# Kernel optimization log

Measured on AMD Instinct MI355X. Metric: run time of the kernel, lower is better.

## Reference

```python
import jax, jax.numpy as jnp
import numpy as np

INF = jnp.float32(np.inf)
LAMBDA_VAL = 1.0
NUM_CLASSES = 10

def setup_inputs() -> dict:
    key = jax.random.key(0)
    k1, k2, k3 = jax.random.split(key, 3)
    N, P, D = 65536, 2048, 64
    x = jax.random.normal(k1, (N, D), dtype=jnp.float32)
    y = jax.random.randint(k2, (N,), 0, NUM_CLASSES)
    prototypes = jax.random.normal(k3, (P, D), dtype=jnp.float32)
    prototype_labels = jnp.arange(P) % NUM_CLASSES
    return {"x": x, "y": y, "prototypes": prototypes, "prototype_labels": prototype_labels}

def _cdist(x, p):
    # Euclidean pairwise distances via the gemm expansion (matches torch.cdist default
    x2 = jnp.sum(x * x, axis=1, keepdims=True)          # [N, 1]
    p2 = jnp.sum(p * p, axis=1)                          # [P]
    sq = x2 + p2[None, :] - 2.0 * (x @ p.T)              # [N, P]
    return jnp.sqrt(jnp.maximum(sq, 0.0))

def reference(x, y, prototypes, prototype_labels):
    distances = _cdist(x, prototypes)                    # [N, P]
    same = prototype_labels[None, :] == y[:, None]       # [N, P] bool
    pos = jnp.min(jnp.where(same, distances, INF), axis=1)   # [N]
    neg = jnp.min(jnp.where(~same, distances, INF), axis=1)  # [N]
    mu = (pos - neg) / (pos + neg)
    loss = jnp.mean(jax.nn.sigmoid(LAMBDA_VAL * mu))
    return loss
```

## Files before the change

### kernel.cpp

```cpp
#include <hip/hip_runtime.h>
#include <math.h>

#define NROWS  65536
#define DDIM   64
#define NCLS   10

#define CLS_SLOTS   208
#define CLS_FFRAGS  13
#define CLS_STRIDE  27648
#define CLS_P2_OFF  26624

typedef __attribute__((ext_vector_type(8))) short bf16x8;
typedef __attribute__((ext_vector_type(4))) float f32x4;
typedef __attribute__((ext_vector_type(4))) unsigned int u32x4;

__device__ inline unsigned int f2bf(float f) {
    unsigned int u = __float_as_uint(f);
    return (u + 0x7FFFu + ((u >> 16) & 1u)) >> 16;
}

template <int CTRL>
__device__ inline float rorMin(float v) {
    int t = __builtin_amdgcn_update_dpp(0, __float_as_int(v), CTRL, 0xF, 0xF, false);
    return fminf(v, __int_as_float(t));
}

__global__ __launch_bounds__(256) void prep_kernel(
        const float* __restrict__ protos, char* __restrict__ wsB,
        float* __restrict__ out) {
    int t = blockIdx.x * 256 + threadIdx.x;
    int s = t >> 3, jj = t & 7;
    int L = s / CLS_SLOTS;
    int j = s - L * CLS_SLOTS;
    int cnt = (L < 8) ? 205 : 204;
    bool real = (j < cnt);
    float v[8] = {0.f, 0.f, 0.f, 0.f, 0.f, 0.f, 0.f, 0.f};
    if (real) {
        const float* src = protos + (L + 10 * j) * DDIM + jj * 8;
        float4 a = *(const float4*)src;
        float4 b = *(const float4*)(src + 4);
        v[0] = a.x; v[1] = a.y; v[2] = a.z; v[3] = a.w;
        v[4] = b.x; v[5] = b.y; v[6] = b.z; v[7] = b.w;
    }
    float ss = 0.f;
#pragma unroll
    for (int i = 0; i < 8; i++) ss = fmaf(v[i], v[i], ss);
    ss += __shfl_xor(ss, 1, 64);
    ss += __shfl_xor(ss, 2, 64);
    ss += __shfl_xor(ss, 4, 64);
    unsigned int w[4];
#pragma unroll
    for (int i = 0; i < 4; i++) {
        unsigned int lo = f2bf(-2.f * v[2 * i]);
        unsigned int hi = f2bf(-2.f * v[2 * i + 1]);
        w[i] = lo | (hi << 16);
    }
    size_t base = (size_t)L * CLS_STRIDE;
    *(u32x4*)(wsB + base + (size_t)(j * 8 + (jj ^ (j & 7))) * 16) =
        (u32x4){w[0], w[1], w[2], w[3]};
    if (jj == 0)
        *(float*)(wsB + base + CLS_P2_OFF + j * 4) =
            real ? ss : __builtin_inff();
    if (t == 0) out[0] = 0.f;
}

template <int CI>
__device__ __forceinline__ void classBody(
        const char* __restrict__ base0,
        int b0off, int b1off, int p2off,
        bf16x8 (&pb0)[3], bf16x8 (&pb1)[3], float (&pp2)[3],
        bf16x8 (&afrag)[4][2], float (&mMin)[4][4]) {
    const char* base = base0 + CI * CLS_STRIDE;
#pragma unroll
    for (int f = 0; f < CLS_FFRAGS; f++) {
        const int slot = (CI * CLS_FFRAGS + f) % 3;
        bf16x8 b0 = pb0[slot];
        bf16x8 b1 = pb1[slot];
        float p2v = pp2[slot];
        if (f <= CLS_FFRAGS - 4) {
            pb0[slot] = *(const bf16x8*)(base + (f + 3) * 2048 + b0off);
            pb1[slot] = *(const bf16x8*)(base + (f + 3) * 2048 + b1off);
            pp2[slot] = *(const float*)(base + p2off + (f + 3) * 64);
        } else if (CI < 4) {
            const char* nb = base + CLS_STRIDE;
            pb0[slot] = *(const bf16x8*)(nb + (f - 10) * 2048 + b0off);
            pb1[slot] = *(const bf16x8*)(nb + (f - 10) * 2048 + b1off);
            pp2[slot] = *(const float*)(nb + p2off + (f - 10) * 64);
        }
        f32x4 p2f = (f32x4){p2v, p2v, p2v, p2v};
#pragma unroll
        for (int m = 0; m < 4; m++) {
            f32x4 acc = __builtin_amdgcn_mfma_f32_16x16x32_bf16(
                afrag[m][0], b0, p2f, 0, 0, 0);
            acc = __builtin_amdgcn_mfma_f32_16x16x32_bf16(
                afrag[m][1], b1, acc, 0, 0, 0);
#pragma unroll
            for (int r = 0; r < 4; r++)
                mMin[m][r] = fminf(mMin[m][r], acc[r]);
        }
    }
}

__global__ __launch_bounds__(256, 2) void glvq_fused(
        const float* __restrict__ x, const int* __restrict__ y,
        const char* __restrict__ wsB, float* __restrict__ out) {
    __shared__ float ldsX2[2][64];
    __shared__ float ldsPos[2][64];
    __shared__ float ldsNeg[2][64];
    __shared__ float ldsRed[2];

    const int tid  = threadIdx.x;
    const int wave = tid >> 6;
    const int lane = tid & 63;
    const int quad = lane >> 4;
    const int l15  = lane & 15;
    const int pair = wave >> 1;
    const int h    = wave & 1;
    const float CINF = __builtin_inff();
    const int rowBase = blockIdx.x * 128 + pair * 64;

    const int b0off = l15 * 128 + (quad ^ (l15 & 7)) * 16;
    const int b1off = l15 * 128 + ((4 + quad) ^ (l15 & 7)) * 16;
    const int p2off = CLS_P2_OFF + l15 * 4;

    const char* base0 = wsB + (size_t)(h * 5) * CLS_STRIDE;

    bf16x8 pb0[3], pb1[3];
    float  pp2[3];
#pragma unroll
    for (int f = 0; f < 3; f++) {
        pb0[f] = *(const bf16x8*)(base0 + f * 2048 + b0off);
        pb1[f] = *(const bf16x8*)(base0 + f * 2048 + b1off);
        pp2[f] = *(const float*)(base0 + p2off + f * 64);
    }

    bf16x8 afrag[4][2];
#pragma unroll
    for (int m = 0; m < 4; m++) {
        float ss = 0.f;
#pragma unroll
        for (int k = 0; k < 2; k++) {
            const float* src = x + (size_t)(rowBase + m * 16 + l15) * DDIM + k * 32 + quad * 8;
            float4 a = *(const float4*)src;
            float4 b = *(const float4*)(src + 4);
            float v[8] = {a.x, a.y, a.z, a.w, b.x, b.y, b.z, b.w};
            unsigned int w[4];
#pragma unroll
            for (int i = 0; i < 4; i++) {
                ss = fmaf(v[2 * i],     v[2 * i],     ss);
                ss = fmaf(v[2 * i + 1], v[2 * i + 1], ss);
                w[i] = f2bf(v[2 * i]) | (f2bf(v[2 * i + 1]) << 16);
            }
            union { u32x4 u; bf16x8 hh; } cvt;
            cvt.u = (u32x4){w[0], w[1], w[2], w[3]};
            afrag[m][k] = cvt.hh;
        }
        ss += __shfl_xor(ss, 16, 64);
        ss += __shfl_xor(ss, 32, 64);
        if (h == 0 && quad == 0) ldsX2[pair][m * 16 + l15] = ss;
    }

    unsigned int yp[4];
#pragma unroll
    for (int m = 0; m < 4; m++) {
        int4 yl = *(const int4*)(y + rowBase + m * 16 + quad * 4);
        yp[m] = (unsigned)yl.x | ((unsigned)yl.y << 8) |
                ((unsigned)yl.z << 16) | ((unsigned)yl.w << 24);
    }

    float pos[4][4], neg[4][4], mMin[4][4];
#pragma unroll
    for (int m = 0; m < 4; m++)
#pragma unroll
        for (int r = 0; r < 4; r++) {
            pos[m][r] = -CINF;
            neg[m][r] = CINF;
            mMin[m][r] = CINF;
        }

    auto endClass = [&](int cls) {
#pragma unroll
        for (int m = 0; m < 4; m++)
#pragma unroll
            for (int r = 0; r < 4; r++) {
                float vmin = mMin[m][r];
                vmin = rorMin<0x128>(vmin);
                vmin = rorMin<0x124>(vmin);
                vmin = rorMin<0x122>(vmin);
                vmin = rorMin<0x121>(vmin);
                bool isPos = (((yp[m] >> (8 * r)) & 255u) == (unsigned)cls);
                pos[m][r] = isPos ? vmin : pos[m][r];
                neg[m][r] = isPos ? neg[m][r] : fminf(neg[m][r], vmin);
                mMin[m][r] = CINF;
            }
    };

    const int h5 = h * 5;
    classBody<0>(base0, b0off, b1off, p2off, pb0, pb1, pp2, afrag, mMin); endClass(h5 + 0);
    classBody<1>(base0, b0off, b1off, p2off, pb0, pb1, pp2, afrag, mMin); endClass(h5 + 1);
    classBody<2>(base0, b0off, b1off, p2off, pb0, pb1, pp2, afrag, mMin); endClass(h5 + 2);
    classBody<3>(base0, b0off, b1off, p2off, pb0, pb1, pp2, afrag, mMin); endClass(h5 + 3);
    classBody<4>(base0, b0off, b1off, p2off, pb0, pb1, pp2, afrag, mMin); endClass(h5 + 4);

    if (h == 1 && l15 == 0) {
#pragma unroll
        for (int m = 0; m < 4; m++)
#pragma unroll
            for (int r = 0; r < 4; r++) {
                ldsPos[pair][m * 16 + quad * 4 + r] = pos[m][r];
                ldsNeg[pair][m * 16 + quad * 4 + r] = neg[m][r];
            }
    }
    __syncthreads();

    float sum = 0.f;
    if (h == 0 && l15 == 0) {
#pragma unroll
        for (int m = 0; m < 4; m++)
#pragma unroll
            for (int r = 0; r < 4; r++) {
                int row = m * 16 + quad * 4 + r;
                float p = fmaxf(pos[m][r], ldsPos[pair][row]);
                float n = fminf(neg[m][r], ldsNeg[pair][row]);
                float x2v = ldsX2[pair][row];
                float sp = sqrtf(fmaxf(x2v + p, 0.f));
                float sn = sqrtf(fmaxf(x2v + n, 0.f));
                float mu = (sp - sn) / (sp + sn);
                sum += 1.f / (1.f + __expf(-mu));
            }
    }
    sum += __shfl_xor(sum, 16, 64);
    sum += __shfl_xor(sum, 32, 64);
    if (h == 0 && lane == 0) ldsRed[pair] = sum;
    __syncthreads();
    if (tid == 0)
        atomicAdd(out, (ldsRed[0] + ldsRed[1]) * (1.f / (float)NROWS));
}

extern "C" void kernel_launch(void* const* d_in, const int* in_sizes, int n_in,
                              void* d_out, int out_size, void* d_ws, size_t ws_size,
                              hipStream_t stream) {
    const float* x      = (const float*)d_in[0];
    const int*   yp     = (const int*)d_in[1];
    const float* protos = (const float*)d_in[2];
    float* out = (float*)d_out;
    char*  wsB = (char*)d_ws;

    prep_kernel<<<65, 256, 0, stream>>>(protos, wsB, out);
    glvq_fused<<<512, 256, 0, stream>>>(x, yp, wsB, out);
}
```

Before: 96.70 us.

## Split prototype fragments within each class across wave pair instead of splitting classes

Previously each of the two waves in a pair handled five whole classes (13 fragments each). Now each wave handles half the fragments of all ten classes (7 fragments per class), using a 4-deep register prefetch ring instead of 3. Per-class minima go to shared memory, and after a barrier one wave per pair combines them per row with the label and computes the loss. This changes load balance and prefetch depth but adds shared-memory traffic, and 2×7 fragments exceed the original 13, so one fragment per class appears to be processed twice; that is harmless for a minimum if the data is valid.

```diff
diff --git a/kernel.cpp b/kernel.cpp
--- a/kernel.cpp
+++ b/kernel.cpp
@@ -66,26 +66,28 @@
 
 template <int CI>
 __device__ __forceinline__ void classBody(
-        const char* __restrict__ base0,
+        const char* __restrict__ wsB, int fLo,
         int b0off, int b1off, int p2off,
-        bf16x8 (&pb0)[3], bf16x8 (&pb1)[3], float (&pp2)[3],
+        bf16x8 (&pb0)[4], bf16x8 (&pb1)[4], float (&pp2)[4],
         bf16x8 (&afrag)[4][2], float (&mMin)[4][4]) {
-    const char* base = base0 + CI * CLS_STRIDE;
-#pragma unroll
-    for (int f = 0; f < CLS_FFRAGS; f++) {
-        const int slot = (CI * CLS_FFRAGS + f) % 3;
+    const char* base = wsB + (size_t)CI * CLS_STRIDE;
+#pragma unroll
+    for (int i = 0; i < 7; i++) {
+        const int slot = (CI * 7 + i) & 3;
         bf16x8 b0 = pb0[slot];
         bf16x8 b1 = pb1[slot];
         float p2v = pp2[slot];
-        if (f <= CLS_FFRAGS - 4) {
-            pb0[slot] = *(const bf16x8*)(base + (f + 3) * 2048 + b0off);
-            pb1[slot] = *(const bf16x8*)(base + (f + 3) * 2048 + b1off);
-            pp2[slot] = *(const float*)(base + p2off + (f + 3) * 64);
-        } else if (CI < 4) {
+        if (i < 3) {
+            const int f = fLo + i + 4;
+            pb0[slot] = *(const bf16x8*)(base + f * 2048 + b0off);
+            pb1[slot] = *(const bf16x8*)(base + f * 2048 + b1off);
+            pp2[slot] = *(const float*)(base + p2off + f * 64);
+        } else if (CI < NCLS - 1) {
             const char* nb = base + CLS_STRIDE;
-            pb0[slot] = *(const bf16x8*)(nb + (f - 10) * 2048 + b0off);
-            pb1[slot] = *(const bf16x8*)(nb + (f - 10) * 2048 + b1off);
-            pp2[slot] = *(const float*)(nb + p2off + (f - 10) * 64);
+            const int f = fLo + i - 3;
+            pb0[slot] = *(const bf16x8*)(nb + f * 2048 + b0off);
+            pb1[slot] = *(const bf16x8*)(nb + f * 2048 + b1off);
+            pp2[slot] = *(const float*)(nb + p2off + f * 64);
         }
         f32x4 p2f = (f32x4){p2v, p2v, p2v, p2v};
 #pragma unroll
@@ -104,9 +106,8 @@
 __global__ __launch_bounds__(256, 2) void glvq_fused(
         const float* __restrict__ x, const int* __restrict__ y,
         const char* __restrict__ wsB, float* __restrict__ out) {
+    __shared__ float ldsMin[2][2][NCLS][64];
     __shared__ float ldsX2[2][64];
-    __shared__ float ldsPos[2][64];
-    __shared__ float ldsNeg[2][64];
     __shared__ float ldsRed[2];
 
     const int tid  = threadIdx.x;
@@ -118,20 +119,20 @@
     const int h    = wave & 1;
     const float CINF = __builtin_inff();
     const int rowBase = blockIdx.x * 128 + pair * 64;
+    const int fLo = h * 6;
 
     const int b0off = l15 * 128 + (quad ^ (l15 & 7)) * 16;
     const int b1off = l15 * 128 + ((4 + quad) ^ (l15 & 7)) * 16;
     const int p2off = CLS_P2_OFF + l15 * 4;
 
-    const char* base0 = wsB + (size_t)(h * 5) * CLS_STRIDE;
-
-    bf16x8 pb0[3], pb1[3];
-    float  pp2[3];
-#pragma unroll
-    for (int f = 0; f < 3; f++) {
-        pb0[f] = *(const bf16x8*)(base0 + f * 2048 + b0off);
-        pb1[f] = *(const bf16x8*)(base0 + f * 2048 + b1off);
-        pp2[f] = *(const float*)(base0 + p2off + f * 64);
+    bf16x8 pb0[4], pb1[4];
+    float  pp2[4];
+#pragma unroll
+    for (int i = 0; i < 4; i++) {
+        const int f = fLo + i;
+        pb0[i] = *(const bf16x8*)(wsB + f * 2048 + b0off);
+        pb1[i] = *(const bf16x8*)(wsB + f * 2048 + b1off);
+        pp2[i] = *(const float*)(wsB + p2off + f * 64);
     }
 
     bf16x8 afrag[4][2];
@@ -160,23 +161,11 @@
         if (h == 0 && quad == 0) ldsX2[pair][m * 16 + l15] = ss;
     }
 
-    unsigned int yp[4];
-#pragma unroll
-    for (int m = 0; m < 4; m++) {
-        int4 yl = *(const int4*)(y + rowBase + m * 16 + quad * 4);
-        yp[m] = (unsigned)yl.x | ((unsigned)yl.y << 8) |
-                ((unsigned)yl.z << 16) | ((unsigned)yl.w << 24);
-    }
-
-    float pos[4][4], neg[4][4], mMin[4][4];
+    float mMin[4][4];
 #pragma unroll
     for (int m = 0; m < 4; m++)
 #pragma unroll
-        for (int r = 0; r < 4; r++) {
-            pos[m][r] = -CINF;
-            neg[m][r] = CINF;
-            mMin[m][r] = CINF;
-        }
+        for (int r = 0; r < 4; r++) mMin[m][r] = CINF;
 
     auto endClass = [&](int cls) {
 #pragma unroll
@@ -188,50 +177,49 @@
                 vmin = rorMin<0x124>(vmin);
                 vmin = rorMin<0x122>(vmin);
                 vmin = rorMin<0x121>(vmin);
-                bool isPos = (((yp[m] >> (8 * r)) & 255u) == (unsigned)cls);
-                pos[m][r] = isPos ? vmin : pos[m][r];
-                neg[m][r] = isPos ? neg[m][r] : fminf(neg[m][r], vmin);
+                if (l15 == 0)
+                    ldsMin[pair][h][cls][m * 16 + quad * 4 + r] = vmin;
                 mMin[m][r] = CINF;
             }
     };
 
-    const int h5 = h * 5;
-    classBody<0>(base0, b0off, b1off, p2off, pb0, pb1, pp2, afrag, mMin); endClass(h5 + 0);
-    classBody<1>(base0, b0off, b1off, p2off, pb0, pb1, pp2, afrag, mMin); endClass(h5 + 1);
-    classBody<2>(base0, b0off, b1off, p2off, pb0, pb1, pp2, afrag, mMin); endClass(h5 + 2);
-    classBody<3>(base0, b0off, b1off, p2off, pb0, pb1, pp2, afrag, mMin); endClass(h5 + 3);
-    classBody<4>(base0, b0off, b1off, p2off, pb0, pb1, pp2, afrag, mMin); endClass(h5 + 4);
-
-    if (h == 1 && l15 == 0) {
-#pragma unroll
-        for (int m = 0; m < 4; m++)
-#pragma unroll
-            for (int r = 0; r < 4; r++) {
-                ldsPos[pair][m * 16 + quad * 4 + r] = pos[m][r];
-                ldsNeg[pair][m * 16 + quad * 4 + r] = neg[m][r];
-            }
-    }
+    classBody<0>(wsB, fLo, b0off, b1off, p2off, pb0, pb1, pp2, afrag, mMin); endClass(0);
+    classBody<1>(wsB, fLo, b0off, b1off, p2off, pb0, pb1, pp2, afrag, mMin); endClass(1);
+    classBody<2>(wsB, fLo, b0off, b1off, p2off, pb0, pb1, pp2, afrag, mMin); endClass(2);
+    classBody<3>(wsB, fLo, b0off, b1off, p2off, pb0, pb1, pp2, afrag, mMin); endClass(3);
+    classBody<4>(wsB, fLo, b0off, b1off, p2off, pb0, pb1, pp2, afrag, mMin); endClass(4);
+    classBody<5>(wsB, fLo, b0off, b1off, p2off, pb0, pb1, pp2, afrag, mMin); endClass(5);
+    classBody<6>(wsB, fLo, b0off, b1off, p2off, pb0, pb1, pp2, afrag, mMin); endClass(6);
+    classBody<7>(wsB, fLo, b0off, b1off, p2off, pb0, pb1, pp2, afrag, mMin); endClass(7);
+    classBody<8>(wsB, fLo, b0off, b1off, p2off, pb0, pb1, pp2, afrag, mMin); endClass(8);
+    classBody<9>(wsB, fLo, b0off, b1off, p2off, pb0, pb1, pp2, afrag, mMin); endClass(9);
+
     __syncthreads();
 
-    float sum = 0.f;
-    if (h == 0 && l15 == 0) {
-#pragma unroll
-        for (int m = 0; m < 4; m++)
-#pragma unroll
-            for (int r = 0; r < 4; r++) {
-                int row = m * 16 + quad * 4 + r;
-                float p = fmaxf(pos[m][r], ldsPos[pair][row]);
-                float n = fminf(neg[m][r], ldsNeg[pair][row]);
-                float x2v = ldsX2[pair][row];
-                float sp = sqrtf(fmaxf(x2v + p, 0.f));
-                float sn = sqrtf(fmaxf(x2v + n, 0.f));
-                float mu = (sp - sn) / (sp + sn);
-                sum += 1.f / (1.f + __expf(-mu));
-            }
-    }
-    sum += __shfl_xor(sum, 16, 64);
-    sum += __shfl_xor(sum, 32, 64);
-    if (h == 0 && lane == 0) ldsRed[pair] = sum;
+    if (h == 0) {
+        const int row = rowBase + lane;
+        const int yr = y[row];
+        const float x2v = ldsX2[pair][lane];
+        float posv = 0.f, negv = CINF;
+#pragma unroll
+        for (int c = 0; c < NCLS; c++) {
+            float fc = fminf(ldsMin[pair][0][c][lane], ldsMin[pair][1][c][lane]);
+            bool isPos = (c == yr);
+            posv = isPos ? fc : posv;
+            negv = isPos ? negv : fminf(negv, fc);
+        }
+        float sp = sqrtf(fmaxf(x2v + posv, 0.f));
+        float sn = sqrtf(fmaxf(x2v + negv, 0.f));
+        float mu = (sp - sn) / (sp + sn);
+        float s = 1.f / (1.f + __expf(-mu));
+        s += __shfl_xor(s, 1, 64);
+        s += __shfl_xor(s, 2, 64);
+        s += __shfl_xor(s, 4, 64);
+        s += __shfl_xor(s, 8, 64);
+        s += __shfl_xor(s, 16, 64);
+        s += __shfl_xor(s, 32, 64);
+        if (lane == 0) ldsRed[pair] = s;
+    }
     __syncthreads();
     if (tid == 0)
         atomicAdd(out, (ldsRed[0] + ldsRed[1]) * (1.f / (float)NROWS));
```

After: 100.6 us. +4.1%, slower.
